# Kernel optimization log

Measured on AMD Instinct MI355X. Metric: run time of the kernel, lower is better.

The kernel has to match this reference:

```python
import math
import jax, jax.numpy as jnp
import numpy as np

S, D, E = 8192, 2048, 64            # tokens, model_dim, num_experts
CAPACITY_FACTOR = 1.0
CAP = int(CAPACITY_FACTOR * math.ceil(S / E))  # 128, static (training-mode 'drop' gate)


def setup_inputs() -> dict:
    key = jax.random.key(0)
    kx, kw = jax.random.split(key)
    x = jax.random.normal(kx, (S, D), dtype=jnp.float32)
    wg = jax.random.normal(kw, (E, D), dtype=jnp.float32) * 0.02  # Linear(D, E, bias=False) weight
    return {"x": x, "wg": wg}


def reference(x, wg):
    # logits = self.wg(input)
    logits = jnp.einsum('sd,ed->se', x, wg)                 # [S, E]
    gates = jax.nn.softmax(logits, axis=1)                  # [S, E]
    indices1_s = jnp.argmax(gates, axis=1)                  # [S]
    mask1 = jax.nn.one_hot(indices1_s, E, dtype=gates.dtype)  # [S, E]

    # load-balancing aux loss
    me = jnp.mean(gates, axis=0)
    ce = jnp.mean(mask1, axis=0)
    l_aux = jnp.mean(me * ce) * (E * E)

    # gates1_s computed BEFORE capacity drop (as in source)
    gates1_s = jnp.sum(gates * mask1, axis=1)               # [S]

    # fused_cumsum_sub_one: position of each token within its expert's queue
    locations1 = jnp.cumsum(mask1, axis=0) - 1.0            # [S, E]
    # capacity drop ('drop' gate type)
    mask1 = mask1 * (locations1 < CAP).astype(mask1.dtype)
    locations1_s = jnp.sum(locations1 * mask1, axis=1).astype(jnp.int32)  # [S]

    gates1 = gates1_s[:, None] * mask1                      # [S, E]
    locations1_sc = jax.nn.one_hot(locations1_s, CAP, dtype=gates1.dtype)  # [S, CAP]
    # bmm(gates1[:,:,None], loc_sc[:,None,:]) == outer product per token
    combine1_sec = jnp.einsum('se,sc->sec', gates1, locations1_sc)  # [S, E, CAP]
    dispatch_mask = combine1_sec.astype(bool)
    return l_aux, combine1_sec, dispatch_mask
```

## Files before the change

kernel.cpp:

```cpp
#include <hip/hip_runtime.h>
#include <cstddef>
#include <cstdint>

#define S_TOK 8192
#define DDIM  2048
#define NEXP  64
#define CAPTY 128
#define KC    64
#define TPB   64
#define NBLK  (S_TOK / TPB)
#define SEC   (S_TOK * NEXP * CAPTY)

__global__ __launch_bounds__(256)
void gate_gemm_kernel(const float* __restrict__ x, const float* __restrict__ wg,
                      float* __restrict__ gate_s, int* __restrict__ expert,
                      int* __restrict__ rank, int* __restrict__ hist,
                      float* __restrict__ partial_g)
{
    __shared__ float xs[KC][TPB + 2];
    __shared__ float ws[KC][NEXP];
    __shared__ float lg[TPB][NEXP + 1];
    __shared__ float smax[TPB];
    __shared__ float srcp[TPB];
    __shared__ int   sexp[TPB];

    const int tid = threadIdx.x;
    const int e4  = tid & 15;
    const int tg  = tid >> 4;
    const int t_base = blockIdx.x * TPB;

    float acc[4][4];
#pragma unroll
    for (int i = 0; i < 4; ++i)
#pragma unroll
        for (int j = 0; j < 4; ++j) acc[i][j] = 0.0f;

    for (int kc = 0; kc < DDIM; kc += KC) {
        __syncthreads();
#pragma unroll
        for (int m = 0; m < 4; ++m) {
            int idx = tid + 256 * m;
            int t = idx & 63;
            int c = idx >> 6;
            float4 v = *(const float4*)(x + (size_t)(t_base + t) * DDIM + kc + c * 4);
            xs[c * 4 + 0][t] = v.x;
            xs[c * 4 + 1][t] = v.y;
            xs[c * 4 + 2][t] = v.z;
            xs[c * 4 + 3][t] = v.w;
            float4 w = *(const float4*)(wg + (size_t)t * DDIM + kc + c * 4);
            ws[c * 4 + 0][t] = w.x;
            ws[c * 4 + 1][t] = w.y;
            ws[c * 4 + 2][t] = w.z;
            ws[c * 4 + 3][t] = w.w;
        }
        __syncthreads();
#pragma unroll 8
        for (int k = 0; k < KC; ++k) {
            float4 wv = *(const float4*)&ws[k][e4 * 4];
            float2 xa = *(const float2*)&xs[k][tg * 4];
            float2 xb = *(const float2*)&xs[k][tg * 4 + 2];
            float xv0 = xa.x, xv1 = xa.y, xv2 = xb.x, xv3 = xb.y;
            acc[0][0] += xv0 * wv.x; acc[0][1] += xv0 * wv.y;
            acc[0][2] += xv0 * wv.z; acc[0][3] += xv0 * wv.w;
            acc[1][0] += xv1 * wv.x; acc[1][1] += xv1 * wv.y;
            acc[1][2] += xv1 * wv.z; acc[1][3] += xv1 * wv.w;
            acc[2][0] += xv2 * wv.x; acc[2][1] += xv2 * wv.y;
            acc[2][2] += xv2 * wv.z; acc[2][3] += xv2 * wv.w;
            acc[3][0] += xv3 * wv.x; acc[3][1] += xv3 * wv.y;
            acc[3][2] += xv3 * wv.z; acc[3][3] += xv3 * wv.w;
        }
    }

    __syncthreads();
#pragma unroll
    for (int i = 0; i < 4; ++i)
#pragma unroll
        for (int j = 0; j < 4; ++j)
            lg[tg * 4 + i][e4 * 4 + j] = acc[i][j];
    __syncthreads();

    if (tid < TPB) {
        int t = tid;
        float m = -1e30f; int am = 0;
        for (int e = 0; e < NEXP; ++e) {
            float v = lg[t][e];
            if (v > m) { m = v; am = e; }
        }
        float s = 0.0f;
        for (int e = 0; e < NEXP; ++e) s += __expf(lg[t][e] - m);
        float rcp = 1.0f / s;
        smax[t] = m; srcp[t] = rcp; sexp[t] = am;
        gate_s[t_base + t] = rcp;
        expert[t_base + t] = am;
    }
    __syncthreads();

    if (tid < TPB) {
        int t = tid;
        int em = sexp[t];
        int r = 0;
        for (int u = 0; u < t; ++u) r += (sexp[u] == em) ? 1 : 0;
        rank[t_base + t] = r;
    }
    if (tid >= 64 && tid < 64 + NEXP) {
        int e = tid - 64;
        float pg = 0.0f; int cnt = 0;
        for (int t = 0; t < TPB; ++t) {
            pg  += __expf(lg[t][e] - smax[t]) * srcp[t];
            cnt += (sexp[t] == e) ? 1 : 0;
        }
        partial_g[blockIdx.x * NEXP + e] = pg;
        hist[blockIdx.x * NEXP + e]      = cnt;
    }
}

__global__ __launch_bounds__(64)
void scan_kernel(const int* __restrict__ hist, const float* __restrict__ partial_g,
                 int* __restrict__ chunk_base, float* __restrict__ out)
{
    int e = threadIdx.x;
    int base = 0;
    float sg = 0.0f;
    for (int c = 0; c < NBLK; ++c) {
        chunk_base[c * NEXP + e] = base;
        base += hist[c * NEXP + e];
        sg   += partial_g[c * NEXP + e];
    }
    float v = sg * (float)base;
#pragma unroll
    for (int off = 32; off > 0; off >>= 1) v += __shfl_down(v, off);
    if (e == 0) {
        out[0] = v * (64.0f / (8192.0f * 8192.0f));
    }
}

__global__ __launch_bounds__(256)
void scatter_kernel(const float* __restrict__ gate_s, const int* __restrict__ expert,
                    const int* __restrict__ rank, const int* __restrict__ chunk_base,
                    float* __restrict__ out)
{
    int s = blockIdx.x * 256 + threadIdx.x;
    if (s >= S_TOK) return;
    int e   = expert[s];
    int loc = chunk_base[(s >> 6) * NEXP + e] + rank[s];
    if (loc < CAPTY) {
        size_t idx = 1 + (size_t)s * (NEXP * CAPTY) + (size_t)e * CAPTY + loc;
        out[idx]       = gate_s[s];
        out[idx + SEC] = 1.0f;
    }
}

extern "C" void kernel_launch(void* const* d_in, const int* in_sizes, int n_in,
                              void* d_out, int out_size, void* d_ws, size_t ws_size,
                              hipStream_t stream)
{
    const float* x  = (const float*)d_in[0];
    const float* wg = (const float*)d_in[1];
    float* out = (float*)d_out;
    char* ws = (char*)d_ws;

    float* gate_s    = (float*)(ws + 0);
    int*   expert    = (int*)  (ws + 32768);
    int*   rank      = (int*)  (ws + 65536);
    int*   hist      = (int*)  (ws + 98304);
    int*   chunk_b   = (int*)  (ws + 131072);
    float* partial_g = (float*)(ws + 163840);

    hipMemsetAsync(d_out, 0, (size_t)out_size * sizeof(float), stream);

    gate_gemm_kernel<<<NBLK, 256, 0, stream>>>(x, wg, gate_s, expert, rank, hist, partial_g);
    scan_kernel<<<1, 64, 0, stream>>>(hist, partial_g, chunk_b, out);
    scatter_kernel<<<(S_TOK + 255) / 256, 256, 0, stream>>>(gate_s, expert, rank, chunk_b, out);
}
```

Measured before the change: 668.1 us.

## Split-K the gate GEMM and move softmax into a separate kernel

Splits the reduction dimension of the gate GEMM 8 ways, so the grid grows from 128 to 1024 blocks and fills more of the GPU. Each block writes partial logits to workspace, and a new softmax kernel sums the partials, computes the softmax, argmax, rank and per-chunk statistics. It also swaps hipMemsetAsync for a custom float4 zero-fill kernel on the large output. The cost is extra workspace traffic for the partials (16 MB) and one more kernel launch.

```diff
diff --git a/kernel.cpp b/kernel.cpp
--- a/kernel.cpp
+++ b/kernel.cpp
@@ -9,25 +9,37 @@
 #define KC    64
 #define TPB   64
 #define NBLK  (S_TOK / TPB)
+#define SPLITK 8
+#define KPER  (DDIM / SPLITK)
 #define SEC   (S_TOK * NEXP * CAPTY)
+
+__global__ __launch_bounds__(256)
+void fill_zero_kernel(float* __restrict__ out)
+{
+    const size_t n4 = (size_t)SEC / 2;
+    float4* out4 = (float4*)out;
+    size_t i = (size_t)blockIdx.x * 256 + threadIdx.x;
+    const size_t stride = (size_t)gridDim.x * 256;
+    float4 z = make_float4(0.f, 0.f, 0.f, 0.f);
+    for (size_t idx = i; idx < n4; idx += stride)
+        out4[idx] = z;
+    if (i == 0) out[(size_t)2 * SEC] = 0.0f;
+}
 
 __global__ __launch_bounds__(256)
 void gate_gemm_kernel(const float* __restrict__ x, const float* __restrict__ wg,
-                      float* __restrict__ gate_s, int* __restrict__ expert,
-                      int* __restrict__ rank, int* __restrict__ hist,
-                      float* __restrict__ partial_g)
+                      float* __restrict__ part)
 {
     __shared__ float xs[KC][TPB + 2];
     __shared__ float ws[KC][NEXP];
-    __shared__ float lg[TPB][NEXP + 1];
-    __shared__ float smax[TPB];
-    __shared__ float srcp[TPB];
-    __shared__ int   sexp[TPB];
 
     const int tid = threadIdx.x;
     const int e4  = tid & 15;
     const int tg  = tid >> 4;
-    const int t_base = blockIdx.x * TPB;
+    const int kp  = blockIdx.x & (SPLITK - 1);
+    const int tc  = blockIdx.x >> 3;
+    const int t_base = tc * TPB;
+    const int k_base = kp * KPER;
 
     float acc[4][4];
 #pragma unroll
@@ -35,7 +47,8 @@
 #pragma unroll
         for (int j = 0; j < 4; ++j) acc[i][j] = 0.0f;
 
-    for (int kc = 0; kc < DDIM; kc += KC) {
+    for (int kc0 = 0; kc0 < KPER; kc0 += KC) {
+        const int kc = k_base + kc0;
         __syncthreads();
 #pragma unroll
         for (int m = 0; m < 4; ++m) {
@@ -71,43 +84,66 @@
         }
     }
 
+#pragma unroll
+    for (int i = 0; i < 4; ++i) {
+        float4 v = make_float4(acc[i][0], acc[i][1], acc[i][2], acc[i][3]);
+        *(float4*)(part + ((size_t)kp * S_TOK + t_base + tg * 4 + i) * NEXP + e4 * 4) = v;
+    }
+}
+
+__global__ __launch_bounds__(64)
+void softmax_kernel(const float* __restrict__ part,
+                    float* __restrict__ gate_s, int* __restrict__ expert,
+                    int* __restrict__ rank, int* __restrict__ hist,
+                    float* __restrict__ partial_g)
+{
+    __shared__ float probs[TPB][NEXP + 1];
+    __shared__ int   sexp[TPB];
+
+    const int t   = threadIdx.x;
+    const int tok = blockIdx.x * TPB + t;
+
+    float lg[NEXP];
+#pragma unroll
+    for (int e = 0; e < NEXP; e += 4) {
+        float4 v = *(const float4*)(part + (size_t)tok * NEXP + e);
+        lg[e] = v.x; lg[e + 1] = v.y; lg[e + 2] = v.z; lg[e + 3] = v.w;
+    }
+#pragma unroll
+    for (int kp = 1; kp < SPLITK; ++kp) {
+#pragma unroll
+        for (int e = 0; e < NEXP; e += 4) {
+            float4 v = *(const float4*)(part + ((size_t)kp * S_TOK + tok) * NEXP + e);
+            lg[e] += v.x; lg[e + 1] += v.y; lg[e + 2] += v.z; lg[e + 3] += v.w;
+        }
+    }
+
+    float m = -1e30f; int am = 0;
+#pragma unroll
+    for (int e = 0; e < NEXP; ++e)
+        if (lg[e] > m) { m = lg[e]; am = e; }
+    float s = 0.0f;
+#pragma unroll
+    for (int e = 0; e < NEXP; ++e) { float p = __expf(lg[e] - m); lg[e] = p; s += p; }
+    float rcp = 1.0f / s;
+#pragma unroll
+    for (int e = 0; e < NEXP; ++e) probs[t][e] = lg[e] * rcp;
+
+    sexp[t] = am;
+    gate_s[tok] = rcp;
+    expert[tok] = am;
     __syncthreads();
-#pragma unroll
-    for (int i = 0; i < 4; ++i)
-#pragma unroll
-        for (int j = 0; j < 4; ++j)
-            lg[tg * 4 + i][e4 * 4 + j] = acc[i][j];
-    __syncthreads();
-
-    if (tid < TPB) {
-        int t = tid;
-        float m = -1e30f; int am = 0;
-        for (int e = 0; e < NEXP; ++e) {
-            float v = lg[t][e];
-            if (v > m) { m = v; am = e; }
-        }
-        float s = 0.0f;
-        for (int e = 0; e < NEXP; ++e) s += __expf(lg[t][e] - m);
-        float rcp = 1.0f / s;
-        smax[t] = m; srcp[t] = rcp; sexp[t] = am;
-        gate_s[t_base + t] = rcp;
-        expert[t_base + t] = am;
-    }
-    __syncthreads();
-
-    if (tid < TPB) {
-        int t = tid;
-        int em = sexp[t];
-        int r = 0;
-        for (int u = 0; u < t; ++u) r += (sexp[u] == em) ? 1 : 0;
-        rank[t_base + t] = r;
-    }
-    if (tid >= 64 && tid < 64 + NEXP) {
-        int e = tid - 64;
+
+    int r = 0;
+    for (int u = 0; u < t; ++u) r += (sexp[u] == am) ? 1 : 0;
+    rank[tok] = r;
+
+    {
+        int e = t;
         float pg = 0.0f; int cnt = 0;
-        for (int t = 0; t < TPB; ++t) {
-            pg  += __expf(lg[t][e] - smax[t]) * srcp[t];
-            cnt += (sexp[t] == e) ? 1 : 0;
+        for (int u = 0; u < TPB; ++u) {
+            pg  += probs[u][e];
+            cnt += (sexp[u] == e) ? 1 : 0;
         }
         partial_g[blockIdx.x * NEXP + e] = pg;
         hist[blockIdx.x * NEXP + e]      = cnt;
@@ -129,9 +165,8 @@
     float v = sg * (float)base;
 #pragma unroll
     for (int off = 32; off > 0; off >>= 1) v += __shfl_down(v, off);
-    if (e == 0) {
+    if (e == 0)
         out[0] = v * (64.0f / (8192.0f * 8192.0f));
-    }
 }
 
 __global__ __launch_bounds__(256)
@@ -159,16 +194,18 @@
     float* out = (float*)d_out;
     char* ws = (char*)d_ws;
 
-    float* gate_s    = (float*)(ws + 0);
-    int*   expert    = (int*)  (ws + 32768);
-    int*   rank      = (int*)  (ws + 65536);
-    int*   hist      = (int*)  (ws + 98304);
-    int*   chunk_b   = (int*)  (ws + 131072);
-    float* partial_g = (float*)(ws + 163840);
-
-    hipMemsetAsync(d_out, 0, (size_t)out_size * sizeof(float), stream);
-
-    gate_gemm_kernel<<<NBLK, 256, 0, stream>>>(x, wg, gate_s, expert, rank, hist, partial_g);
+    float* part      = (float*)(ws + 0);
+    size_t off = (size_t)SPLITK * S_TOK * NEXP * sizeof(float);
+    float* gate_s    = (float*)(ws + off);          off += 32768;
+    int*   expert    = (int*)  (ws + off);          off += 32768;
+    int*   rank      = (int*)  (ws + off);          off += 32768;
+    int*   hist      = (int*)  (ws + off);          off += 32768;
+    int*   chunk_b   = (int*)  (ws + off);          off += 32768;
+    float* partial_g = (float*)(ws + off);
+
+    fill_zero_kernel<<<4096, 256, 0, stream>>>(out);
+    gate_gemm_kernel<<<NBLK * SPLITK, 256, 0, stream>>>(x, wg, part);
+    softmax_kernel<<<NBLK, 64, 0, stream>>>(part, gate_s, expert, rank, hist, partial_g);
     scan_kernel<<<1, 64, 0, stream>>>(hist, partial_g, chunk_b, out);
     scatter_kernel<<<(S_TOK + 255) / 256, 256, 0, stream>>>(gate_s, expert, rank, chunk_b, out);
 }
```

Result: faster. 630.8 us (-5.6%).
